# Performance work log

Hardware: AMD Instinct MI355X
Metric: run time of the kernel (lower is better)

The kernel has to match this reference:

```python
import jax, jax.numpy as jnp
import numpy as np

N, D = 8192, 256

def setup_inputs() -> dict:
    key = jax.random.key(0)
    k1, k2 = jax.random.split(key)
    data = jnp.zeros((1,), dtype=jnp.float32)  # unused by the module
    Z = jax.random.normal(k1, (N, D), dtype=jnp.float32)
    A_hat = jax.random.uniform(k2, (N, N), dtype=jnp.float32)
    return {"data": data, "Z": Z, "A_hat": A_hat}

def reference(data, Z, A_hat):
    A = A_hat.astype(jnp.float32)
    # D^{-1/2} A D^{-1/2}: diagonal matmuls are mathematically row/col scaling
    d_inv_sqrt = 1.0 / jnp.sqrt(A.sum(axis=1) + 1e-10)  # [N]
    A_norm = A * d_inv_sqrt[:, None] * d_inv_sqrt[None, :]  # [N, N]
    # cosine similarity (F.normalize uses eps=1e-12 clamp on the norm)
    z_norm = jnp.linalg.norm(Z, axis=1, keepdims=True)
    Z_n = Z / jnp.maximum(z_norm, 1e-12)
    similarity = Z_n @ Z_n.T  # [N, N]
    homo_loss = -jnp.sum(A_norm * similarity)
    hetero_loss = jnp.sum((1.0 - A_norm) * similarity)
    return (homo_loss, hetero_loss)
```

## Files before the change

kernel.cpp:

```cpp
#include <hip/hip_runtime.h>
#include <hip/hip_fp16.h>

typedef _Float16 f16x8  __attribute__((ext_vector_type(8)));
typedef _Float16 f16x4  __attribute__((ext_vector_type(4)));
typedef float    f32x16 __attribute__((ext_vector_type(16)));

constexpr int Nn = 8192;
constexpr int Dd = 256;

constexpr int BM = 64;
constexpr int KC = 1024;
constexpr int SK = 64;
constexpr int NSC = KC / SK;

__global__ __launch_bounds__(256) void k_rowsum(const float* __restrict__ A,
                                                float* __restrict__ dis,
                                                float* __restrict__ rd,
                                                float* __restrict__ T) {
    if (blockIdx.x == 0 && threadIdx.x == 0) *T = 0.f;
    const int row  = blockIdx.x * 4 + (threadIdx.x >> 6);
    const int lane = threadIdx.x & 63;
    const float4* rp = reinterpret_cast<const float4*>(A + (size_t)row * Nn);
    float s = 0.f;
    #pragma unroll
    for (int i = 0; i < Nn / 256; ++i) {
        float4 v = rp[i * 64 + lane];
        s += (v.x + v.y) + (v.z + v.w);
    }
    #pragma unroll
    for (int off = 32; off > 0; off >>= 1) s += __shfl_down(s, off, 64);
    if (lane == 0) {
        float rs = s + 1e-10f;
        dis[row] = rsqrtf(rs);
        rd[row]  = sqrtf(rs);
    }
}

__global__ __launch_bounds__(256) void k_makeYt(const float* __restrict__ Z,
                                               const float* __restrict__ dis,
                                               _Float16* __restrict__ Yt,
                                               _Float16* __restrict__ Yr) {
    __shared__ float nrm[64][4];
    __shared__ _Float16 tile[Dd][72];
    const int t = threadIdx.x;
    const int r = t >> 2, q = t & 3;
    const int row = blockIdx.x * 64 + r;
    const float4* zp = reinterpret_cast<const float4*>(Z + (size_t)row * Dd + q * 64);
    float4 v[16];
    float ss = 0.f;
    #pragma unroll
    for (int i = 0; i < 16; ++i) {
        v[i] = zp[i];
        ss += v[i].x*v[i].x + v[i].y*v[i].y + v[i].z*v[i].z + v[i].w*v[i].w;
    }
    nrm[r][q] = ss;
    __syncthreads();
    const float tot   = nrm[r][0] + nrm[r][1] + nrm[r][2] + nrm[r][3];
    const float scale = dis[row] / fmaxf(sqrtf(tot), 1e-12f);
    #pragma unroll
    for (int i = 0; i < 16; ++i) {
        const int c0 = q * 64 + i * 4;
        f16x4 y = { (_Float16)(v[i].x * scale), (_Float16)(v[i].y * scale),
                    (_Float16)(v[i].z * scale), (_Float16)(v[i].w * scale) };
        tile[c0+0][r] = y[0];
        tile[c0+1][r] = y[1];
        tile[c0+2][r] = y[2];
        tile[c0+3][r] = y[3];
        *reinterpret_cast<f16x4*>(Yr + (size_t)row * Dd + c0) = y;
    }
    __syncthreads();
    int4*       dst = reinterpret_cast<int4*>(Yt + (size_t)t * Nn + blockIdx.x * 64);
    const int4* src = reinterpret_cast<const int4*>(&tile[t][0]);
    #pragma unroll
    for (int i = 0; i < 8; ++i) dst[i] = src[i];
}

__global__ __launch_bounds__(256) void k_colsum(const _Float16* __restrict__ Yt,
                                                const float* __restrict__ rd,
                                                float* __restrict__ s) {
    const int k = blockIdx.x;
    const int t = threadIdx.x;
    const _Float16* yp = Yt + (size_t)k * Nn + t * 32;
    const float*    rp = rd + t * 32;
    float acc = 0.f;
    #pragma unroll
    for (int i = 0; i < 32; ++i) acc += (float)yp[i] * rp[i];
    #pragma unroll
    for (int off = 32; off > 0; off >>= 1) acc += __shfl_down(acc, off, 64);
    __shared__ float red[4];
    if ((t & 63) == 0) red[t >> 6] = acc;
    __syncthreads();
    if (t == 0) s[k] = red[0] + red[1] + red[2] + red[3];
}

__global__ __launch_bounds__(512, 4) void k_main(const float* __restrict__ A,
                                                 const _Float16* __restrict__ Yt,
                                                 const _Float16* __restrict__ Yr,
                                                 float* __restrict__ T) {
    __shared__ _Float16 Ys[2 * Dd * SK];

    const int ib = blockIdx.x & (Nn / BM - 1);
    const int jb = blockIdx.x >> 7;
    const int I0 = ib * BM;
    const int K0 = jb * KC;
    const int w   = threadIdx.x >> 6;
    const int wm  = w & 1;
    const int wn  = (w >> 1) & 1;
    const int wk  = w >> 2;
    const int l   = threadIdx.x & 63;
    const int ln  = l & 31;
    const int lkh = l >> 5;

    const size_t arow = (size_t)(I0 + wm * 32 + ln) * Nn;
    const int    koff = wk * 32 + lkh * 8;

    f32x16 acc[4];
    #pragma unroll
    for (int t = 0; t < 4; ++t) acc[t] = (f32x16)(0.f);

    #define STAGE(SC, BUF)                                                     \
    {   const int kc = K0 + (SC) * SK;                                         \
        _Pragma("unroll")                                                      \
        for (int q = 0; q < 4; ++q) {                                          \
            const int nrow = w * 32 + q * 8 + (l >> 3);                        \
            const int s8   = (l & 7) ^ (l >> 3);                               \
            __builtin_amdgcn_global_load_lds(                                  \
                (const __attribute__((address_space(1))) unsigned int*)        \
                    (Yt + (size_t)nrow * Nn + kc + s8 * 8),                    \
                (__attribute__((address_space(3))) unsigned int*)              \
                    (Ys + (BUF) * (Dd * SK) + (w * 32 + q * 8) * SK),          \
                16, 0, 0);                                                     \
        }                                                                      \
    }

    float4 av[4];
    #define LOADA(SC)                                                          \
    {   const float* ab = A + arow + K0 + (SC) * SK + koff;                    \
        av[0] = *reinterpret_cast<const float4*>(ab);                          \
        av[1] = *reinterpret_cast<const float4*>(ab + 4);                      \
        av[2] = *reinterpret_cast<const float4*>(ab + 16);                     \
        av[3] = *reinterpret_cast<const float4*>(ab + 20);                     \
    }

    STAGE(0, 0);
    LOADA(0);
    asm volatile("s_waitcnt vmcnt(0)" ::: "memory");
    __builtin_amdgcn_s_barrier();

    for (int sc = 0; sc < NSC; ++sc) {
        const int cur = sc & 1;
        f16x8 af[2];
        #pragma unroll
        for (int ks = 0; ks < 2; ++ks) {
            const float4 a0 = av[ks*2], a1 = av[ks*2+1];
            af[ks] = f16x8{ (_Float16)a0.x, (_Float16)a0.y, (_Float16)a0.z, (_Float16)a0.w,
                            (_Float16)a1.x, (_Float16)a1.y, (_Float16)a1.z, (_Float16)a1.w };
        }
        if (sc + 1 < NSC) {
            STAGE(sc + 1, cur ^ 1);
            LOADA(sc + 1);
        }
        #pragma unroll
        for (int tn = 0; tn < 4; ++tn) {
            const int n = wn * 128 + tn * 32 + ln;
            #pragma unroll
            for (int ks = 0; ks < 2; ++ks) {
                const int sl = (wk * 4 + ks * 2 + lkh) ^ (n & 7);
                const f16x8 bf = *reinterpret_cast<const f16x8*>(
                    Ys + cur * (Dd * SK) + n * SK + sl * 8);
                acc[tn] = __builtin_amdgcn_mfma_f32_32x32x16_f16(af[ks], bf, acc[tn], 0, 0, 0);
            }
        }
        if (sc + 1 < NSC) {
            asm volatile("s_waitcnt vmcnt(4)" ::: "memory");
            __builtin_amdgcn_s_barrier();
        }
    }

    float part = 0.f;
    #pragma unroll
    for (int tn = 0; tn < 4; ++tn) {
        const int n = wn * 128 + tn * 32 + ln;
        #pragma unroll
        for (int r = 0; r < 16; ++r) {
            const int i = I0 + wm * 32 + (r & 3) + 8 * (r >> 2) + 4 * lkh;
            part += acc[tn][r] * (float)Yr[(size_t)i * Dd + n];
        }
    }
    #pragma unroll
    for (int off = 32; off > 0; off >>= 1) part += __shfl_down(part, off, 64);
    __shared__ float red[8];
    if (l == 0) red[w] = part;
    __syncthreads();
    if (threadIdx.x == 0) {
        float t = 0.f;
        #pragma unroll
        for (int i = 0; i < 8; ++i) t += red[i];
        atomicAdd(T, t);
    }
}

__global__ __launch_bounds__(256) void k_final(const float* __restrict__ s,
                                               const float* __restrict__ T,
                                               float* __restrict__ out) {
    const int t = threadIdx.x;
    float v = s[t];
    float p = v * v;
    #pragma unroll
    for (int off = 32; off > 0; off >>= 1) p += __shfl_down(p, off, 64);
    __shared__ float red[4];
    if ((t & 63) == 0) red[t >> 6] = p;
    __syncthreads();
    if (t == 0) {
        const float ss = red[0] + red[1] + red[2] + red[3];
        const float Tv = *T;
        out[0] = -Tv;
        out[1] = ss - Tv;
    }
}

extern "C" void kernel_launch(void* const* d_in, const int* in_sizes, int n_in,
                              void* d_out, int out_size, void* d_ws, size_t ws_size,
                              hipStream_t stream) {
    const float* Z = (const float*)d_in[1];
    const float* A = (const float*)d_in[2];
    float* out = (float*)d_out;

    char* ws = (char*)d_ws;
    float*    dis = (float*)(ws);
    float*    rd  = (float*)(ws + 32768);
    float*    s   = (float*)(ws + 65536);
    float*    T   = (float*)(ws + 66560);
    _Float16* Yt  = (_Float16*)(ws + 131072);
    _Float16* Yr  = (_Float16*)(ws + 131072 + (size_t)Nn * Dd * 2);

    k_rowsum<<<Nn / 4, 256, 0, stream>>>(A, dis, rd, T);
    k_makeYt<<<Nn / 64, 256, 0, stream>>>(Z, dis, Yt, Yr);
    k_colsum<<<Dd, 256, 0, stream>>>(Yt, rd, s);
    k_main<<<(Nn / BM) * (Nn / KC), 512, 0, stream>>>(A, Yt, Yr, T);
    k_final<<<1, 256, 0, stream>>>(s, T, out);
}
```

Before: 148.2 us.

## Enlarge main tile to 256 rows with 1024-thread blocks and split K halves

The main kernel moves from 64-row tiles with 512 threads, where the K chunk was split across warp groups, to 256-row tiles with 16 waves of 1024 threads. Each wave now walks the whole 64-wide K step in two halves, with A loads and conversions interleaved between the MFMA halves. The point is to reuse each staged Yt tile in shared memory across four times as many rows, cutting redundant Yt traffic, and to overlap A loads with compute. In exchange the grid shrinks to 256 blocks, one per CU, and the launch-bounds occupancy hint is dropped, which may leave less latency hiding.

```diff
diff --git a/kernel.cpp b/kernel.cpp
--- a/kernel.cpp
+++ b/kernel.cpp
@@ -8,7 +8,7 @@
 constexpr int Nn = 8192;
 constexpr int Dd = 256;
 
-constexpr int BM = 64;
+constexpr int BM = 256;
 constexpr int KC = 1024;
 constexpr int SK = 64;
 constexpr int NSC = KC / SK;
@@ -93,26 +93,24 @@
     if (t == 0) s[k] = red[0] + red[1] + red[2] + red[3];
 }
 
-__global__ __launch_bounds__(512, 4) void k_main(const float* __restrict__ A,
-                                                 const _Float16* __restrict__ Yt,
-                                                 const _Float16* __restrict__ Yr,
-                                                 float* __restrict__ T) {
+__global__ __launch_bounds__(1024) void k_main(const float* __restrict__ A,
+                                               const _Float16* __restrict__ Yt,
+                                               const _Float16* __restrict__ Yr,
+                                               float* __restrict__ T) {
     __shared__ _Float16 Ys[2 * Dd * SK];
 
     const int ib = blockIdx.x & (Nn / BM - 1);
-    const int jb = blockIdx.x >> 7;
+    const int jb = blockIdx.x >> 5;
     const int I0 = ib * BM;
     const int K0 = jb * KC;
     const int w   = threadIdx.x >> 6;
-    const int wm  = w & 1;
-    const int wn  = (w >> 1) & 1;
-    const int wk  = w >> 2;
+    const int wm  = w >> 1;
+    const int wn  = w & 1;
     const int l   = threadIdx.x & 63;
     const int ln  = l & 31;
     const int lkh = l >> 5;
 
     const size_t arow = (size_t)(I0 + wm * 32 + ln) * Nn;
-    const int    koff = wk * 32 + lkh * 8;
 
     f32x16 acc[4];
     #pragma unroll
@@ -121,56 +119,67 @@
     #define STAGE(SC, BUF)                                                     \
     {   const int kc = K0 + (SC) * SK;                                         \
         _Pragma("unroll")                                                      \
-        for (int q = 0; q < 4; ++q) {                                          \
-            const int nrow = w * 32 + q * 8 + (l >> 3);                        \
+        for (int q = 0; q < 2; ++q) {                                          \
+            const int nrow = w * 16 + q * 8 + (l >> 3);                        \
             const int s8   = (l & 7) ^ (l >> 3);                               \
             __builtin_amdgcn_global_load_lds(                                  \
                 (const __attribute__((address_space(1))) unsigned int*)        \
                     (Yt + (size_t)nrow * Nn + kc + s8 * 8),                    \
                 (__attribute__((address_space(3))) unsigned int*)              \
-                    (Ys + (BUF) * (Dd * SK) + (w * 32 + q * 8) * SK),          \
+                    (Ys + (BUF) * (Dd * SK) + (w * 16 + q * 8) * SK),          \
                 16, 0, 0);                                                     \
         }                                                                      \
     }
 
     float4 av[4];
-    #define LOADA(SC)                                                          \
-    {   const float* ab = A + arow + K0 + (SC) * SK + koff;                    \
+    #define LOADA(SC, H)                                                       \
+    {   const float* ab = A + arow + K0 + (SC) * SK + (H) * 32 + lkh * 8;      \
         av[0] = *reinterpret_cast<const float4*>(ab);                          \
         av[1] = *reinterpret_cast<const float4*>(ab + 4);                      \
         av[2] = *reinterpret_cast<const float4*>(ab + 16);                     \
         av[3] = *reinterpret_cast<const float4*>(ab + 20);                     \
     }
 
+    #define CVT(AF)                                                            \
+    {   const float4 a0 = av[0], a1 = av[1], a2 = av[2], a3 = av[3];           \
+        AF[0] = f16x8{ (_Float16)a0.x, (_Float16)a0.y, (_Float16)a0.z,         \
+                       (_Float16)a0.w, (_Float16)a1.x, (_Float16)a1.y,         \
+                       (_Float16)a1.z, (_Float16)a1.w };                       \
+        AF[1] = f16x8{ (_Float16)a2.x, (_Float16)a2.y, (_Float16)a2.z,         \
+                       (_Float16)a2.w, (_Float16)a3.x, (_Float16)a3.y,         \
+                       (_Float16)a3.z, (_Float16)a3.w };                       \
+    }
+
+    #define HALF(CUR, H, AF)                                                   \
+    {   _Pragma("unroll")                                                      \
+        for (int tn = 0; tn < 4; ++tn) {                                       \
+            const int n = wn * 128 + tn * 32 + ln;                             \
+            _Pragma("unroll")                                                  \
+            for (int ks = 0; ks < 2; ++ks) {                                   \
+                const int sl = ((H) * 4 + ks * 2 + lkh) ^ (n & 7);             \
+                const f16x8 bf = *reinterpret_cast<const f16x8*>(              \
+                    Ys + (CUR) * (Dd * SK) + n * SK + sl * 8);                 \
+                acc[tn] = __builtin_amdgcn_mfma_f32_32x32x16_f16(              \
+                    AF[ks], bf, acc[tn], 0, 0, 0);                             \
+            }                                                                  \
+        }                                                                      \
+    }
+
     STAGE(0, 0);
-    LOADA(0);
+    LOADA(0, 0);
     asm volatile("s_waitcnt vmcnt(0)" ::: "memory");
     __builtin_amdgcn_s_barrier();
 
     for (int sc = 0; sc < NSC; ++sc) {
         const int cur = sc & 1;
-        f16x8 af[2];
-        #pragma unroll
-        for (int ks = 0; ks < 2; ++ks) {
-            const float4 a0 = av[ks*2], a1 = av[ks*2+1];
-            af[ks] = f16x8{ (_Float16)a0.x, (_Float16)a0.y, (_Float16)a0.z, (_Float16)a0.w,
-                            (_Float16)a1.x, (_Float16)a1.y, (_Float16)a1.z, (_Float16)a1.w };
-        }
-        if (sc + 1 < NSC) {
-            STAGE(sc + 1, cur ^ 1);
-            LOADA(sc + 1);
-        }
-        #pragma unroll
-        for (int tn = 0; tn < 4; ++tn) {
-            const int n = wn * 128 + tn * 32 + ln;
-            #pragma unroll
-            for (int ks = 0; ks < 2; ++ks) {
-                const int sl = (wk * 4 + ks * 2 + lkh) ^ (n & 7);
-                const f16x8 bf = *reinterpret_cast<const f16x8*>(
-                    Ys + cur * (Dd * SK) + n * SK + sl * 8);
-                acc[tn] = __builtin_amdgcn_mfma_f32_32x32x16_f16(af[ks], bf, acc[tn], 0, 0, 0);
-            }
-        }
+        f16x8 af0[2], af1[2];
+        CVT(af0);
+        LOADA(sc, 1);
+        if (sc + 1 < NSC) STAGE(sc + 1, cur ^ 1);
+        HALF(cur, 0, af0);
+        CVT(af1);
+        if (sc + 1 < NSC) LOADA(sc + 1, 0);
+        HALF(cur, 1, af1);
         if (sc + 1 < NSC) {
             asm volatile("s_waitcnt vmcnt(4)" ::: "memory");
             __builtin_amdgcn_s_barrier();
@@ -189,13 +198,13 @@
     }
     #pragma unroll
     for (int off = 32; off > 0; off >>= 1) part += __shfl_down(part, off, 64);
-    __shared__ float red[8];
+    __shared__ float red[16];
     if (l == 0) red[w] = part;
     __syncthreads();
     if (threadIdx.x == 0) {
         float t = 0.f;
         #pragma unroll
-        for (int i = 0; i < 8; ++i) t += red[i];
+        for (int i = 0; i < 16; ++i) t += red[i];
         atomicAdd(T, t);
     }
 }
@@ -237,6 +246,6 @@
     k_rowsum<<<Nn / 4, 256, 0, stream>>>(A, dis, rd, T);
     k_makeYt<<<Nn / 64, 256, 0, stream>>>(Z, dis, Yt, Yr);
     k_colsum<<<Dd, 256, 0, stream>>>(Yt, rd, s);
-    k_main<<<(Nn / BM) * (Nn / KC), 512, 0, stream>>>(A, Yt, Yr, T);
+    k_main<<<(Nn / BM) * (Nn / KC), 1024, 0, stream>>>(A, Yt, Yr, T);
     k_final<<<1, 256, 0, stream>>>(s, T, out);
 }
```

Result: faster. 136.2 us (-8.1%).

## Stage A tiles through LDS with triple-buffered async loads and larger row tiles

Applied to the files above, without the earlier changes.

The main GEMM-like kernel now works on 256-row blocks with 1024 threads and a 32-wide k step. Both A (fp32) and Yt tiles are fetched with direct global-to-LDS loads into a three-deep ring, instead of loading A into registers and double-buffering only Y. The larger row block means each Y tile is reused across four times as many rows, which cuts Y traffic, and the deeper pipeline hides more memory latency. In exchange LDS use and block size go up, which may lower occupancy, and the k-split removes the old wk split so each wave issues more MFMAs per stage.

```diff
diff --git a/kernel.cpp b/kernel.cpp
--- a/kernel.cpp
+++ b/kernel.cpp
@@ -8,10 +8,12 @@
 constexpr int Nn = 8192;
 constexpr int Dd = 256;
 
-constexpr int BM = 64;
+constexpr int BM = 256;
 constexpr int KC = 1024;
-constexpr int SK = 64;
+constexpr int SK = 32;
 constexpr int NSC = KC / SK;
+constexpr int ABUF = BM * SK;
+constexpr int YBUF = Dd * SK;
 
 __global__ __launch_bounds__(256) void k_rowsum(const float* __restrict__ A,
                                                 float* __restrict__ dis,
@@ -93,87 +95,87 @@
     if (t == 0) s[k] = red[0] + red[1] + red[2] + red[3];
 }
 
-__global__ __launch_bounds__(512, 4) void k_main(const float* __restrict__ A,
-                                                 const _Float16* __restrict__ Yt,
-                                                 const _Float16* __restrict__ Yr,
-                                                 float* __restrict__ T) {
-    __shared__ _Float16 Ys[2 * Dd * SK];
+__global__ __launch_bounds__(1024, 4) void k_main(const float* __restrict__ A,
+                                                  const _Float16* __restrict__ Yt,
+                                                  const _Float16* __restrict__ Yr,
+                                                  float* __restrict__ T) {
+    __shared__ float    As[3 * ABUF];
+    __shared__ _Float16 Ysm[3 * YBUF];
 
     const int ib = blockIdx.x & (Nn / BM - 1);
-    const int jb = blockIdx.x >> 7;
+    const int jb = blockIdx.x >> 5;
     const int I0 = ib * BM;
     const int K0 = jb * KC;
-    const int w   = threadIdx.x >> 6;
-    const int wm  = w & 1;
-    const int wn  = (w >> 1) & 1;
-    const int wk  = w >> 2;
-    const int l   = threadIdx.x & 63;
+    const int t   = threadIdx.x;
+    const int w   = t >> 6;
+    const int wm  = w >> 1;
+    const int wn  = w & 1;
+    const int l   = t & 63;
     const int ln  = l & 31;
     const int lkh = l >> 5;
 
-    const size_t arow = (size_t)(I0 + wm * 32 + ln) * Nn;
-    const int    koff = wk * 32 + lkh * 8;
-
     f32x16 acc[4];
     #pragma unroll
-    for (int t = 0; t < 4; ++t) acc[t] = (f32x16)(0.f);
-
-    #define STAGE(SC, BUF)                                                     \
+    for (int q = 0; q < 4; ++q) acc[q] = (f32x16)(0.f);
+
+    #define STAGE(SC, B)                                                       \
     {   const int kc = K0 + (SC) * SK;                                         \
+        const int ga = (l & 7) ^ (l >> 3);                                     \
         _Pragma("unroll")                                                      \
-        for (int q = 0; q < 4; ++q) {                                          \
-            const int nrow = w * 32 + q * 8 + (l >> 3);                        \
-            const int s8   = (l & 7) ^ (l >> 3);                               \
+        for (int q = 0; q < 2; ++q) {                                          \
+            const int row = q * 128 + w * 8 + (l >> 3);                        \
             __builtin_amdgcn_global_load_lds(                                  \
                 (const __attribute__((address_space(1))) unsigned int*)        \
-                    (Yt + (size_t)nrow * Nn + kc + s8 * 8),                    \
+                    (A + (size_t)(I0 + row) * Nn + kc + ga * 4),               \
                 (__attribute__((address_space(3))) unsigned int*)              \
-                    (Ys + (BUF) * (Dd * SK) + (w * 32 + q * 8) * SK),          \
+                    (As + (B) * ABUF + (q * 128 + w * 8) * SK),                \
                 16, 0, 0);                                                     \
         }                                                                      \
-    }
-
-    float4 av[4];
-    #define LOADA(SC)                                                          \
-    {   const float* ab = A + arow + K0 + (SC) * SK + koff;                    \
-        av[0] = *reinterpret_cast<const float4*>(ab);                          \
-        av[1] = *reinterpret_cast<const float4*>(ab + 4);                      \
-        av[2] = *reinterpret_cast<const float4*>(ab + 16);                     \
-        av[3] = *reinterpret_cast<const float4*>(ab + 20);                     \
+        const int gy = (l & 3) ^ ((l >> 3) & 3);                               \
+        const int nr = w * 16 + (l >> 2);                                      \
+        __builtin_amdgcn_global_load_lds(                                      \
+            (const __attribute__((address_space(1))) unsigned int*)            \
+                (Yt + (size_t)nr * Nn + kc + gy * 8),                          \
+            (__attribute__((address_space(3))) unsigned int*)                  \
+                (Ysm + (B) * YBUF + (w * 16) * SK),                            \
+            16, 0, 0);                                                         \
     }
 
     STAGE(0, 0);
-    LOADA(0);
-    asm volatile("s_waitcnt vmcnt(0)" ::: "memory");
-    __builtin_amdgcn_s_barrier();
+    STAGE(1, 1);
 
     for (int sc = 0; sc < NSC; ++sc) {
-        const int cur = sc & 1;
+        if (sc + 1 < NSC) { asm volatile("s_waitcnt vmcnt(3)" ::: "memory"); }
+        else              { asm volatile("s_waitcnt vmcnt(0)" ::: "memory"); }
+        __builtin_amdgcn_s_barrier();
+        if (sc + 2 < NSC) {
+            const int b2 = (sc + 2) % 3;
+            STAGE(sc + 2, b2);
+        }
+        const int cb = sc % 3;
+        const float*    Ab = As  + cb * ABUF + (wm * 32 + ln) * SK;
+        const _Float16* Yb = Ysm + cb * YBUF;
+        const int r7 = ln & 7;
         f16x8 af[2];
         #pragma unroll
         for (int ks = 0; ks < 2; ++ks) {
-            const float4 a0 = av[ks*2], a1 = av[ks*2+1];
-            af[ks] = f16x8{ (_Float16)a0.x, (_Float16)a0.y, (_Float16)a0.z, (_Float16)a0.w,
-                            (_Float16)a1.x, (_Float16)a1.y, (_Float16)a1.z, (_Float16)a1.w };
-        }
-        if (sc + 1 < NSC) {
-            STAGE(sc + 1, cur ^ 1);
-            LOADA(sc + 1);
+            const int s0 = ks * 4 + lkh * 2;
+            const float4 u0 = *reinterpret_cast<const float4*>(Ab + ((s0)     ^ r7) * 4);
+            const float4 u1 = *reinterpret_cast<const float4*>(Ab + ((s0 + 1) ^ r7) * 4);
+            af[ks] = f16x8{ (_Float16)u0.x, (_Float16)u0.y, (_Float16)u0.z, (_Float16)u0.w,
+                            (_Float16)u1.x, (_Float16)u1.y, (_Float16)u1.z, (_Float16)u1.w };
         }
         #pragma unroll
         for (int tn = 0; tn < 4; ++tn) {
             const int n = wn * 128 + tn * 32 + ln;
+            const _Float16* Yrow = Yb + n * SK;
+            const int sw = (ln >> 1) & 3;
             #pragma unroll
             for (int ks = 0; ks < 2; ++ks) {
-                const int sl = (wk * 4 + ks * 2 + lkh) ^ (n & 7);
-                const f16x8 bf = *reinterpret_cast<const f16x8*>(
-                    Ys + cur * (Dd * SK) + n * SK + sl * 8);
+                const int tt = (ks * 2 + lkh) ^ sw;
+                const f16x8 bf = *reinterpret_cast<const f16x8*>(Yrow + tt * 8);
                 acc[tn] = __builtin_amdgcn_mfma_f32_32x32x16_f16(af[ks], bf, acc[tn], 0, 0, 0);
             }
-        }
-        if (sc + 1 < NSC) {
-            asm volatile("s_waitcnt vmcnt(4)" ::: "memory");
-            __builtin_amdgcn_s_barrier();
         }
     }
 
@@ -189,14 +191,14 @@
     }
     #pragma unroll
     for (int off = 32; off > 0; off >>= 1) part += __shfl_down(part, off, 64);
-    __shared__ float red[8];
+    __shared__ float red[16];
     if (l == 0) red[w] = part;
     __syncthreads();
     if (threadIdx.x == 0) {
-        float t = 0.f;
-        #pragma unroll
-        for (int i = 0; i < 8; ++i) t += red[i];
-        atomicAdd(T, t);
+        float tt = 0.f;
+        #pragma unroll
+        for (int i = 0; i < 16; ++i) tt += red[i];
+        atomicAdd(T, tt);
     }
 }
 
@@ -237,6 +239,6 @@
     k_rowsum<<<Nn / 4, 256, 0, stream>>>(A, dis, rd, T);
     k_makeYt<<<Nn / 64, 256, 0, stream>>>(Z, dis, Yt, Yr);
     k_colsum<<<Dd, 256, 0, stream>>>(Yt, rd, s);
-    k_main<<<(Nn / BM) * (Nn / KC), 512, 0, stream>>>(A, Yt, Yr, T);
+    k_main<<<(Nn / BM) * (Nn / KC), 1024, 0, stream>>>(A, Yt, Yr, T);
     k_final<<<1, 256, 0, stream>>>(s, T, out);
 }
```

Measured after the change: 126.6 us. 1.17x faster.
